# Performance work log

Hardware: AMD Instinct MI355X
Metric: run time of the kernel (lower is better)

The kernel has to match this reference:

```python
import jax, jax.numpy as jnp
import numpy as np

# Locally-connected 2D convolution (torch legacy SpatialConvolutionLocal)
# out[b,o,h,w] = sum_{c,i,j} weight[h,w,o,c,i,j] * x_pad[b,c,h*dH+i,w*dW+j] + bias[o,h,w]

B, CIN, IH, IW = 32, 32, 64, 64
COUT, KH, KW = 64, 3, 3
DH, DW = 1, 1
PADH, PADW = 1, 1
OH = (IH + 2 * PADH - KH) // DH + 1
OW = (IW + 2 * PADW - KW) // DW + 1


def setup_inputs() -> dict:
    key = jax.random.key(0)
    k1, k2, k3 = jax.random.split(key, 3)
    stdv = 1.0 / np.sqrt(KW * KH * CIN)
    x = jax.random.normal(k1, (B, CIN, IH, IW), dtype=jnp.float32)
    weight = jax.random.uniform(k2, (OH, OW, COUT, CIN, KH, KW), dtype=jnp.float32,
                                minval=-stdv, maxval=stdv)
    bias = jax.random.uniform(k3, (COUT, OH, OW), dtype=jnp.float32,
                              minval=-stdv, maxval=stdv)
    return {"x": x, "weight": weight, "bias": bias}


def _extract_patches(x):
    # x: [B, C, IH, IW] -> patches [B, C, KH, KW, OH, OW]
    xp = jnp.pad(x, ((0, 0), (0, 0), (PADH, PADH), (PADW, PADW)))
    rows = []
    for i in range(KH):  # small fixed kernel loop (9 iters), not a data-dim loop
        cols = []
        for j in range(KW):
            cols.append(xp[:, :, i:i + OH * DH:DH, j:j + OW * DW:DW])
        rows.append(jnp.stack(cols, axis=2))  # [B, C, KW, OH, OW]
    return jnp.stack(rows, axis=2)  # [B, C, KH, KW, OH, OW]


def reference(x, weight, bias):
    patches = _extract_patches(x)  # [B, C, KH, KW, OH, OW]
    # per-position GEMM: distinct weight matrix at each (h, w)
    out = jnp.einsum('bcijhw,hwocij->bohw', patches, weight)
    return out + bias[None]  # [B, COUT, OH, OW]
```

## Files before the change

### kernel.cpp

```cpp
#include <hip/hip_runtime.h>


#define KP 88

typedef __attribute__((ext_vector_type(8))) short short8;
typedef __attribute__((ext_vector_type(16))) float f32x16;

__device__ __forceinline__ unsigned f2bf(float f) {
    unsigned u = __builtin_bit_cast(unsigned, f);
    return (u + 0x7FFFu + ((u >> 16) & 1u)) >> 16;
}

__global__ __launch_bounds__(256, 3) void lcconv_kernel(
    const float* __restrict__ xg,
    const float* __restrict__ wg,
    const float* __restrict__ bg,
    float* __restrict__ outg)
{
    __shared__ unsigned short Wl[4 * 32 * KP];
    __shared__ unsigned short Pl[4 * 32 * KP];

    const int tid = threadIdx.x;
    const int bid = blockIdx.x;
    const int oh = bid & 1;
    const int ws = (bid >> 1) & 15;
    const int h  = bid >> 5;
    const int w0 = ws * 4;
    const int og = oh * 32;

    {
        unsigned short* base = (tid & 128) ? Pl : Wl;
        int row = tid & 127;
        *(short8*)(base + row * KP + 72) = (short8)0;
    }

    f32x16 acc;
#pragma unroll
    for (int i = 0; i < 16; i++) acc[i] = 0.f;

    const int lane = tid & 63;
    const int wv   = tid >> 6;
    const int mrow = lane & 31;
    const int g    = lane >> 5;

    float4 wreg[9];
    float2 xreg[12];

#pragma unroll
    for (int it = 0; it < 9; it++) {
        int f4 = it * 256 + tid;
        int run = f4 / 18, within = f4 - run * 18;
        int p = run >> 5, o = run & 31;
        wreg[it] = *(const float4*)(
            wg + ((h * 64 + (w0 + p)) * 64 + og + o) * 288 + within * 4);
    }
#pragma unroll
    for (int it = 0; it < 12; it++) {
        int task = it * 256 + tid;
        int f2i = task & 3, row = task >> 2;
        int b = row / 24, rem = row - b * 24;
        int c = rem / 3, y3 = rem - c * 3;
        int y = h + y3 - 1;
        int gx0 = w0 - 2 + 2 * f2i;
        if ((unsigned)y < 64u && (unsigned)gx0 < 64u)
            xreg[it] = *(const float2*)(xg + ((b * 32 + c) * 64 + y) * 64 + gx0);
        else
            xreg[it] = float2{0.f, 0.f};
    }

    for (int cc = 0; cc < 4; cc++) {
        __syncthreads();

#pragma unroll
        for (int it = 0; it < 9; it++) {
            int f4 = it * 256 + tid;
            int run = f4 / 18, within = f4 - run * 18;
            float4 w4 = wreg[it];
            unsigned long long pk = (unsigned long long)f2bf(w4.x)
                | ((unsigned long long)f2bf(w4.y) << 16)
                | ((unsigned long long)f2bf(w4.z) << 32)
                | ((unsigned long long)f2bf(w4.w) << 48);
            *(unsigned long long*)(Wl + run * KP + within * 4) = pk;
        }

#pragma unroll
        for (int it = 0; it < 12; it++) {
            int task = it * 256 + tid;
            int f2i = task & 3, row = task >> 2;
            int b = row / 24, rem = row - b * 24;
            int c = rem / 3, y3 = rem - c * 3;
            int kb = c * 9 + y3 * 3;
            int pb = b * KP + kb;
            unsigned bx0 = f2bf(xreg[it].x);
            unsigned bx1 = f2bf(xreg[it].y);
#pragma unroll
            for (int q = 0; q < 2; q++) {
                int xc = f2i * 2 + q;
                unsigned short bv = (unsigned short)(q ? bx1 : bx0);
#pragma unroll
                for (int j = 0; j < 3; j++) {
                    int p = xc - 1 - j;
                    if ((unsigned)p < 4u)
                        Pl[p * (32 * KP) + pb + j] = bv;
                }
            }
        }
        __syncthreads();

        if (cc < 3) {
            const int c0n = (cc + 1) * 8;
#pragma unroll
            for (int it = 0; it < 9; it++) {
                int f4 = it * 256 + tid;
                int run = f4 / 18, within = f4 - run * 18;
                int p = run >> 5, o = run & 31;
                wreg[it] = *(const float4*)(
                    wg + ((h * 64 + (w0 + p)) * 64 + og + o) * 288 + c0n * 9 + within * 4);
            }
#pragma unroll
            for (int it = 0; it < 12; it++) {
                int task = it * 256 + tid;
                int f2i = task & 3, row = task >> 2;
                int b = row / 24, rem = row - b * 24;
                int c = rem / 3, y3 = rem - c * 3;
                int y = h + y3 - 1;
                int gx0 = w0 - 2 + 2 * f2i;
                if ((unsigned)y < 64u && (unsigned)gx0 < 64u)
                    xreg[it] = *(const float2*)(xg + ((b * 32 + c0n + c) * 64 + y) * 64 + gx0);
                else
                    xreg[it] = float2{0.f, 0.f};
            }
        }

#pragma unroll
        for (int ks = 0; ks < 5; ks++) {
            short8 a  = *(const short8*)(Pl + (wv * 32 + mrow) * KP + ks * 16 + g * 8);
            short8 b8 = *(const short8*)(Wl + (wv * 32 + mrow) * KP + ks * 16 + g * 8);
            acc = __builtin_amdgcn_mfma_f32_32x32x16_bf16(a, b8, acc, 0, 0, 0);
        }
    }
    __syncthreads();

    float* outl = (float*)Wl;
#pragma unroll
    for (int r = 0; r < 16; r++) {
        int row = (r & 3) + 8 * (r >> 2) + 4 * g;
        outl[(wv * 32 + row) * 32 + mrow] = acc[r];
    }
    __syncthreads();

#pragma unroll
    for (int it = 0; it < 4; it++) {
        int id = it * 256 + tid;
        int b = id >> 5;
        int o = id & 31;
        float4 v;
        v.x = outl[0 * 1024 + b * 32 + o];
        v.y = outl[1 * 1024 + b * 32 + o];
        v.z = outl[2 * 1024 + b * 32 + o];
        v.w = outl[3 * 1024 + b * 32 + o];
        const float4 bb = *(const float4*)(bg + ((og + o) * 64 + h) * 64 + w0);
        v.x += bb.x; v.y += bb.y; v.z += bb.z; v.w += bb.w;
        *(float4*)(outg + ((b * 64 + og + o) * 64 + h) * 64 + w0) = v;
    }
}

extern "C" void kernel_launch(void* const* d_in, const int* in_sizes, int n_in,
                              void* d_out, int out_size, void* d_ws, size_t ws_size,
                              hipStream_t stream) {
    const float* x = (const float*)d_in[0];
    const float* w = (const float*)d_in[1];
    const float* b = (const float*)d_in[2];
    float* out = (float*)d_out;
    lcconv_kernel<<<dim3(2048), dim3(256), 0, stream>>>(x, w, b, out);
}
```

Measured before the change: 510.8 us.

## Load weights straight into MFMA B-fragment registers and double-buffer the patch tile

Weights no longer go through shared memory. Each lane loads its own B-fragment rows from global memory and converts them to bf16 in registers, prefetching the next channel chunk while the MFMAs run. The patch tile now uses a fragment-friendly shared layout with two buffers, so each chunk needs only one barrier. Blocks are remapped for locality and launch bounds move to 4 blocks per CU. The trade-offs are higher register pressure and some reads past the 72-element chunk boundary, which are clamped and multiplied by zeroed A padding.

```diff
diff --git a/kernel.cpp b/kernel.cpp
--- a/kernel.cpp
+++ b/kernel.cpp
@@ -1,9 +1,12 @@
 #include <hip/hip_runtime.h>
 
 
-#define KP 88
+#define NP 4
+#define KU 10
+#define PLBUF (NP * KU * 256)
 
 typedef __attribute__((ext_vector_type(8))) short short8;
+typedef __attribute__((ext_vector_type(4))) int int4v;
 typedef __attribute__((ext_vector_type(16))) float f32x16;
 
 __device__ __forceinline__ unsigned f2bf(float f) {
@@ -11,49 +14,17 @@
     return (u + 0x7FFFu + ((u >> 16) & 1u)) >> 16;
 }
 
-__global__ __launch_bounds__(256, 3) void lcconv_kernel(
-    const float* __restrict__ xg,
-    const float* __restrict__ wg,
-    const float* __restrict__ bg,
-    float* __restrict__ outg)
-{
-    __shared__ unsigned short Wl[4 * 32 * KP];
-    __shared__ unsigned short Pl[4 * 32 * KP];
+__device__ __forceinline__ short8 cvt8(float4 a, float4 b) {
+    int4v r;
+    r.x = (int)(f2bf(a.x) | (f2bf(a.y) << 16));
+    r.y = (int)(f2bf(a.z) | (f2bf(a.w) << 16));
+    r.z = (int)(f2bf(b.x) | (f2bf(b.y) << 16));
+    r.w = (int)(f2bf(b.z) | (f2bf(b.w) << 16));
+    return __builtin_bit_cast(short8, r);
+}
 
-    const int tid = threadIdx.x;
-    const int bid = blockIdx.x;
-    const int oh = bid & 1;
-    const int ws = (bid >> 1) & 15;
-    const int h  = bid >> 5;
-    const int w0 = ws * 4;
-    const int og = oh * 32;
-
-    {
-        unsigned short* base = (tid & 128) ? Pl : Wl;
-        int row = tid & 127;
-        *(short8*)(base + row * KP + 72) = (short8)0;
-    }
-
-    f32x16 acc;
-#pragma unroll
-    for (int i = 0; i < 16; i++) acc[i] = 0.f;
-
-    const int lane = tid & 63;
-    const int wv   = tid >> 6;
-    const int mrow = lane & 31;
-    const int g    = lane >> 5;
-
-    float4 wreg[9];
-    float2 xreg[12];
-
-#pragma unroll
-    for (int it = 0; it < 9; it++) {
-        int f4 = it * 256 + tid;
-        int run = f4 / 18, within = f4 - run * 18;
-        int p = run >> 5, o = run & 31;
-        wreg[it] = *(const float4*)(
-            wg + ((h * 64 + (w0 + p)) * 64 + og + o) * 288 + within * 4);
-    }
+__device__ __forceinline__ void load_x(const float* __restrict__ xg, int h, int w0,
+                                       int tid, int c0, float2* xreg) {
 #pragma unroll
     for (int it = 0; it < 12; it++) {
         int task = it * 256 + tid;
@@ -63,85 +34,110 @@
         int y = h + y3 - 1;
         int gx0 = w0 - 2 + 2 * f2i;
         if ((unsigned)y < 64u && (unsigned)gx0 < 64u)
-            xreg[it] = *(const float2*)(xg + ((b * 32 + c) * 64 + y) * 64 + gx0);
+            xreg[it] = *(const float2*)(xg + ((b * 32 + c0 + c) * 64 + y) * 64 + gx0);
         else
             xreg[it] = float2{0.f, 0.f};
     }
+}
 
-    for (int cc = 0; cc < 4; cc++) {
-        __syncthreads();
-
+__device__ __forceinline__ void fanout(unsigned short* Plb, int tid, const float2* xreg) {
 #pragma unroll
-        for (int it = 0; it < 9; it++) {
-            int f4 = it * 256 + tid;
-            int run = f4 / 18, within = f4 - run * 18;
-            float4 w4 = wreg[it];
-            unsigned long long pk = (unsigned long long)f2bf(w4.x)
-                | ((unsigned long long)f2bf(w4.y) << 16)
-                | ((unsigned long long)f2bf(w4.z) << 32)
-                | ((unsigned long long)f2bf(w4.w) << 48);
-            *(unsigned long long*)(Wl + run * KP + within * 4) = pk;
-        }
-
+    for (int it = 0; it < 12; it++) {
+        int task = it * 256 + tid;
+        int f2i = task & 3, row = task >> 2;
+        int b = row / 24, rem = row - b * 24;
+        int c = rem / 3, y3 = rem - c * 3;
+        int kb = c * 9 + y3 * 3;
+        unsigned bx0 = f2bf(xreg[it].x), bx1 = f2bf(xreg[it].y);
 #pragma unroll
-        for (int it = 0; it < 12; it++) {
-            int task = it * 256 + tid;
-            int f2i = task & 3, row = task >> 2;
-            int b = row / 24, rem = row - b * 24;
-            int c = rem / 3, y3 = rem - c * 3;
-            int kb = c * 9 + y3 * 3;
-            int pb = b * KP + kb;
-            unsigned bx0 = f2bf(xreg[it].x);
-            unsigned bx1 = f2bf(xreg[it].y);
+        for (int qq = 0; qq < 2; qq++) {
+            int xc = f2i * 2 + qq;
+            unsigned short bv = (unsigned short)(qq ? bx1 : bx0);
 #pragma unroll
-            for (int q = 0; q < 2; q++) {
-                int xc = f2i * 2 + q;
-                unsigned short bv = (unsigned short)(q ? bx1 : bx0);
-#pragma unroll
-                for (int j = 0; j < 3; j++) {
-                    int p = xc - 1 - j;
-                    if ((unsigned)p < 4u)
-                        Pl[p * (32 * KP) + pb + j] = bv;
+            for (int j = 0; j < 3; j++) {
+                int p = xc - 1 - j;
+                if ((unsigned)p < 4u) {
+                    int k = kb + j;
+                    Plb[(p * KU + (k >> 3)) * 256 + b * 8 + (k & 7)] = bv;
                 }
             }
         }
-        __syncthreads();
+    }
+}
 
-        if (cc < 3) {
-            const int c0n = (cc + 1) * 8;
+__global__ __launch_bounds__(256, 4) void lcconv_kernel(
+    const float* __restrict__ xg,
+    const float* __restrict__ wg,
+    const float* __restrict__ bg,
+    float* __restrict__ outg)
+{
+    __shared__ unsigned short Pl[2 * PLBUF];
+
+    const int tid = threadIdx.x;
+    const int bid = blockIdx.x;
+    const int xr = bid & 7;
+    const int q  = bid >> 3;
+    const int s  = q & 3;
+    const int u  = ((q >> 2) << 3) | xr;
+    const int h  = u >> 3;
+    const int t  = (u & 7) >> 1;
+    const int oh = u & 1;
+    const int w0 = (t * 4 + s) * 4;
+    const int og = oh * 32;
+
+    const int lane = tid & 63;
+    const int wv   = tid >> 6;
+    const int mrow = lane & 31;
+    const int g    = lane >> 5;
+
+    {
+        int bufp = tid >> 7;
+        int rp   = tid & 127;
+        int p = rp >> 5, b = rp & 31;
+        *(short8*)&Pl[bufp * PLBUF + ((p * KU + 9) * 32 + b) * 8] = (short8)0;
+    }
+
+    f32x16 acc;
 #pragma unroll
-            for (int it = 0; it < 9; it++) {
-                int f4 = it * 256 + tid;
-                int run = f4 / 18, within = f4 - run * 18;
-                int p = run >> 5, o = run & 31;
-                wreg[it] = *(const float4*)(
-                    wg + ((h * 64 + (w0 + p)) * 64 + og + o) * 288 + c0n * 9 + within * 4);
-            }
+    for (int i = 0; i < 16; i++) acc[i] = 0.f;
+
+    const float4* wrow = (const float4*)(wg + (((h * 64 + w0 + wv) * 64) + og + mrow) * 288);
+
+    float4 breg[5][2];
+    float2 xreg[12];
+
+    load_x(xg, h, w0, tid, 0, xreg);
 #pragma unroll
-            for (int it = 0; it < 12; it++) {
-                int task = it * 256 + tid;
-                int f2i = task & 3, row = task >> 2;
-                int b = row / 24, rem = row - b * 24;
-                int c = rem / 3, y3 = rem - c * 3;
-                int y = h + y3 - 1;
-                int gx0 = w0 - 2 + 2 * f2i;
-                if ((unsigned)y < 64u && (unsigned)gx0 < 64u)
-                    xreg[it] = *(const float2*)(xg + ((b * 32 + c0n + c) * 64 + y) * 64 + gx0);
-                else
-                    xreg[it] = float2{0.f, 0.f};
-            }
-        }
+    for (int ks = 0; ks < 5; ks++) {
+        int fo = ks * 4 + g * 2;
+        breg[ks][0] = wrow[fo];
+        breg[ks][1] = wrow[fo + 1];
+    }
 
 #pragma unroll
+    for (int cc = 0; cc < 4; cc++) {
+        unsigned short* Plb = Pl + (cc & 1) * PLBUF;
+        fanout(Plb, tid, xreg);
+        __syncthreads();
+        if (cc < 3) load_x(xg, h, w0, tid, (cc + 1) * 8, xreg);
+
+        const unsigned short* Arow = Plb + (wv * KU) * 256 + mrow * 8;
+#pragma unroll
         for (int ks = 0; ks < 5; ks++) {
-            short8 a  = *(const short8*)(Pl + (wv * 32 + mrow) * KP + ks * 16 + g * 8);
-            short8 b8 = *(const short8*)(Wl + (wv * 32 + mrow) * KP + ks * 16 + g * 8);
-            acc = __builtin_amdgcn_mfma_f32_32x32x16_bf16(a, b8, acc, 0, 0, 0);
+            short8 afrag = *(const short8*)(Arow + (ks * 2 + g) * 256);
+            short8 bfrag = cvt8(breg[ks][0], breg[ks][1]);
+            if (cc < 3) {
+                int fo = (cc + 1) * 18 + ks * 4 + g * 2;
+                fo = fo > 70 ? 70 : fo;
+                int fo1 = fo + 1 > 71 ? 71 : fo + 1;
+                breg[ks][0] = wrow[fo];
+                breg[ks][1] = wrow[fo1];
+            }
+            acc = __builtin_amdgcn_mfma_f32_32x32x16_bf16(afrag, bfrag, acc, 0, 0, 0);
         }
     }
-    __syncthreads();
 
-    float* outl = (float*)Wl;
+    float* outl = (float*)Pl;
 #pragma unroll
     for (int r = 0; r < 16; r++) {
         int row = (r & 3) + 8 * (r >> 2) + 4 * g;
@@ -152,8 +148,7 @@
 #pragma unroll
     for (int it = 0; it < 4; it++) {
         int id = it * 256 + tid;
-        int b = id >> 5;
-        int o = id & 31;
+        int b = id >> 5, o = id & 31;
         float4 v;
         v.x = outl[0 * 1024 + b * 32 + o];
         v.y = outl[1 * 1024 + b * 32 + o];
```

Result: slower. 705.6 us (+38.2%).
